# Kernel tuning notes

Hardware: AMD Instinct MI355X
Metric: run time of the kernel (lower is better)

## Reference

```python
import jax, jax.numpy as jnp
import numpy as np

NUM_HEADS = 8
N_POINTS = 9
OFFSET_SCALE = 4.0


def bilinear_sample(fmap_flat, xy, H, W):
    """fmap_flat: (BH, H*W, C) row-major spatial; xy: (BH, S, 2) pixel coords (x, y).
    grid_sample(mode='bilinear', padding_mode='zeros', align_corners=True) equivalent.
    Returns (BH, S, C)."""
    x, y = xy[..., 0], xy[..., 1]
    x0 = jnp.floor(x); y0 = jnp.floor(y)
    x1 = x0 + 1.0;    y1 = y0 + 1.0
    wx1 = x - x0; wx0 = 1.0 - wx1
    wy1 = y - y0; wy0 = 1.0 - wy1

    def corner(xi, yi, wgt):
        valid = (xi >= 0) & (xi <= W - 1) & (yi >= 0) & (yi <= H - 1)
        xi_c = jnp.clip(xi, 0, W - 1).astype(jnp.int32)
        yi_c = jnp.clip(yi, 0, H - 1).astype(jnp.int32)
        idx = yi_c * W + xi_c                                   # (BH, S)
        vals = jnp.take_along_axis(fmap_flat, idx[..., None], axis=1)  # (BH, S, C)
        return vals * (wgt * valid.astype(fmap_flat.dtype))[..., None]

    return (corner(x0, y0, wx0 * wy0) + corner(x1, y0, wx1 * wy0)
            + corner(x0, y1, wx0 * wy1) + corner(x1, y1, wx1 * wy1))


def setup_inputs() -> dict:
    key = jax.random.key(0)
    ks = jax.random.split(key, 10)
    B, N, D = 4, 6400, 256
    Hh, P = NUM_HEADS, N_POINTS
    s = 0.02
    return {
        "x":    jax.random.normal(ks[0], (B, N, D), dtype=jnp.float32),
        "Wq":   jax.random.normal(ks[1], (D, D), dtype=jnp.float32) * s,
        "bq":   jnp.zeros((D,), jnp.float32),
        "Woff": jax.random.normal(ks[2], (Hh * P * 2, D), dtype=jnp.float32) * s,
        "boff": jax.random.normal(ks[3], (Hh * P * 2,), dtype=jnp.float32) * s,
        "Wkv":  jax.random.normal(ks[4], (2 * D, D), dtype=jnp.float32) * s,
        "bkv":  jnp.zeros((2 * D,), jnp.float32),
        "Wout": jax.random.normal(ks[5], (D, D), dtype=jnp.float32) * s,
        "bout": jnp.zeros((D,), jnp.float32),
        "h": 40,
        "w": 160,
    }


def reference(x, Wq, bq, Woff, boff, Wkv, bkv, Wout, bout, h, w):
    B, N, D = x.shape
    H, P = NUM_HEADS, N_POINTS
    hd = D // H

    # queries: (B, H, N, hd)
    q = (x @ Wq.T + bq).reshape(B, N, H, hd).transpose(0, 2, 1, 3)

    # per-query per-head offsets in pixels: (B, N, H, P, 2) (dx, dy)
    offsets = jnp.tanh(x @ Woff.T + boff).reshape(B, N, H, P, 2) * OFFSET_SCALE

    # K/V feature maps via 1x1 conv == per-token linear; split heads, flat spatial
    kv = x @ Wkv.T + bkv                     # (B, N, 2D)
    k = kv[..., :D]
    v = kv[..., D:]
    k_flat = k.reshape(B, N, H, hd).transpose(0, 2, 1, 3).reshape(B * H, N, hd)
    v_flat = v.reshape(B, N, H, hd).transpose(0, 2, 1, 3).reshape(B * H, N, hd)

    # base pixel grid (x, y), row-major over (h, w)
    ys, xs = jnp.meshgrid(jnp.arange(h, dtype=x.dtype), jnp.arange(w, dtype=x.dtype), indexing="ij")
    base_xy = jnp.stack([xs, ys], axis=-1).reshape(N, 2)

    # sampling locations: (B, N, H, P, 2) -> (B*H, N*P, 2)
    sample_xy = base_xy[None, :, None, None, :] + offsets
    sample_xy = sample_xy.transpose(0, 2, 1, 3, 4).reshape(B * H, N * P, 2)

    sampled_k = bilinear_sample(k_flat, sample_xy, h, w).reshape(B, H, N, P, hd)
    sampled_v = bilinear_sample(v_flat, sample_xy, h, w).reshape(B, H, N, P, hd)

    logits = jnp.einsum("bhnd,bhnpd->bhnp", q, sampled_k) * (hd ** -0.5)
    attn = jax.nn.softmax(logits, axis=-1)
    out = jnp.einsum("bhnp,bhnpd->bhnd", attn, sampled_v)   # (B, H, N, hd)
    out = out.transpose(0, 2, 1, 3).reshape(B, N, D)
    return out @ Wout.T + bout
```

## Files before the change

kernel.cpp:

```cpp
#include <hip/hip_runtime.h>
#include <math.h>

#define BSZ    4
#define NTOK   6400
#define DMODEL 256
#define NHEAD  8
#define HDIM   32
#define NPTS   9
#define HSP    40
#define WSP    160
#define KDIM   256
#define MTOT   (BSZ*NTOK)
#define NFUSED 912

typedef short  short8  __attribute__((ext_vector_type(8)));
typedef float  floatx4 __attribute__((ext_vector_type(4)));

__device__ __forceinline__ ushort f2bf(float f) {
    uint u = __float_as_uint(f);
    u = (u + 0x7FFFu + ((u >> 16) & 1u)) >> 16;
    return (ushort)u;
}

__device__ __forceinline__ float fast_tanh(float v) {
    const float e = __expf(2.0f * v);
    return 1.0f - 2.0f / (e + 1.0f);
}

__device__ __forceinline__ void unpack8(uint4 u, float* f) {
    f[0] = __uint_as_float(u.x << 16); f[1] = __uint_as_float(u.x & 0xFFFF0000u);
    f[2] = __uint_as_float(u.y << 16); f[3] = __uint_as_float(u.y & 0xFFFF0000u);
    f[4] = __uint_as_float(u.z << 16); f[5] = __uint_as_float(u.z & 0xFFFF0000u);
    f[6] = __uint_as_float(u.w << 16); f[7] = __uint_as_float(u.w & 0xFFFF0000u);
}

__global__ __launch_bounds__(256) void cast_all(
    const float* __restrict__ x,   const float* __restrict__ Wq,
    const float* __restrict__ Woff,const float* __restrict__ Wkv,
    const float* __restrict__ Wout,
    ushort* __restrict__ xb, ushort* __restrict__ wfused, ushort* __restrict__ woutb)
{
    const int bid = blockIdx.x;
    const float* src; ushort* dst; int base;
    if      (bid < 6400) { src = x;    dst = xb;              base = bid; }
    else if (bid < 6464) { src = Wq;   dst = wfused;          base = bid - 6400; }
    else if (bid < 6500) { src = Woff; dst = wfused + 65536;  base = bid - 6464; }
    else if (bid < 6628) { src = Wkv;  dst = wfused + 102400; base = bid - 6500; }
    else                 { src = Wout; dst = woutb;           base = bid - 6628; }
    const int i = base * 1024 + threadIdx.x * 4;
    float4 v = *(const float4*)(src + i);
    ushort4 o;
    o.x = f2bf(v.x); o.y = f2bf(v.y); o.z = f2bf(v.z); o.w = f2bf(v.w);
    *(ushort4*)(dst + i) = o;
}

template <int MODE>
__global__ __launch_bounds__(256, 3) void gemm_mfma(
    const ushort* __restrict__ Xb,
    const ushort* __restrict__ Wb,
    const float* __restrict__ bq, const float* __restrict__ boff,
    const float* __restrict__ bkv,
    ushort* __restrict__ qb, float* __restrict__ off,
    ushort* __restrict__ kfb, ushort* __restrict__ vfb,
    float* __restrict__ Y)
{
    const int Ncols = (MODE == 0) ? NFUSED : DMODEL;
    __shared__ ushort As[2][128 * 32];
    __shared__ ushort Bs[2][128 * 32];

    const int tid = threadIdx.x;
    const int block_n = blockIdx.x * 128;
    const int block_m = blockIdx.y * 128;
    const int wave = tid >> 6, lane = tid & 63;
    const int wm = (wave >> 1) * 64, wn = (wave & 1) * 64;
    const int l15 = lane & 15, quad = lane >> 4;

    const int r0 = tid >> 2,        q0 = tid & 3;
    const int r1 = (tid + 256) >> 2;
    const int sw0 = ((r0 ^ (r0 >> 2)) & 3);
    const int sw1 = ((r1 ^ (r1 >> 2)) & 3);
    const int lA0 = r0 * 32 + ((q0 ^ sw0) << 3);
    const int lA1 = r1 * 32 + ((q0 ^ sw1) << 3);

    const ushort* gA0 = Xb + (size_t)(block_m + r0) * KDIM + q0 * 8;
    const ushort* gA1 = Xb + (size_t)(block_m + r1) * KDIM + q0 * 8;
    const int bc0 = min(block_n + r0, Ncols - 1);
    const int bc1 = min(block_n + r1, Ncols - 1);
    const ushort* gB0 = Wb + (size_t)bc0 * KDIM + q0 * 8;
    const ushort* gB1 = Wb + (size_t)bc1 * KDIM + q0 * 8;

    const int swf = (l15 & 3) ^ ((l15 >> 2) & 3);
    const int physoff = ((quad ^ swf) << 3);

    floatx4 acc[4][4];
    #pragma unroll
    for (int i = 0; i < 4; ++i)
        #pragma unroll
        for (int j = 0; j < 4; ++j) {
            acc[i][j][0] = 0.f; acc[i][j][1] = 0.f;
            acc[i][j][2] = 0.f; acc[i][j][3] = 0.f;
        }

    {
        uint4 a0 = *(const uint4*)gA0;
        uint4 a1 = *(const uint4*)gA1;
        uint4 b0 = *(const uint4*)gB0;
        uint4 b1 = *(const uint4*)gB1;
        *(uint4*)&As[0][lA0] = a0;  *(uint4*)&As[0][lA1] = a1;
        *(uint4*)&Bs[0][lA0] = b0;  *(uint4*)&Bs[0][lA1] = b1;
    }

    uint4 ra0, ra1, rb0, rb1;
    #pragma unroll
    for (int k8 = 0; k8 < 8; ++k8) {
        __syncthreads();
        if (k8 < 7) {
            const int ko = (k8 + 1) * 32;
            ra0 = *(const uint4*)(gA0 + ko);
            ra1 = *(const uint4*)(gA1 + ko);
            rb0 = *(const uint4*)(gB0 + ko);
            rb1 = *(const uint4*)(gB1 + ko);
        }
        const ushort* Ab = As[k8 & 1];
        const ushort* Bb = Bs[k8 & 1];
        short8 af[4], bfr[4];
        #pragma unroll
        for (int f = 0; f < 4; ++f) {
            af[f]  = *(const short8*)&Ab[(wm + f * 16 + l15) * 32 + physoff];
            bfr[f] = *(const short8*)&Bb[(wn + f * 16 + l15) * 32 + physoff];
        }
        #pragma unroll
        for (int fm = 0; fm < 4; ++fm)
            #pragma unroll
            for (int fn = 0; fn < 4; ++fn)
                acc[fm][fn] = __builtin_amdgcn_mfma_f32_16x16x32_bf16(
                    af[fm], bfr[fn], acc[fm][fn], 0, 0, 0);
        if (k8 < 7) {
            ushort* An = As[(k8 + 1) & 1];
            ushort* Bn = Bs[(k8 + 1) & 1];
            *(uint4*)&An[lA0] = ra0;  *(uint4*)&An[lA1] = ra1;
            *(uint4*)&Bn[lA0] = rb0;  *(uint4*)&Bn[lA1] = rb1;
        }
    }

    float bcol[4]; int colv[4];
    #pragma unroll
    for (int fn = 0; fn < 4; ++fn) {
        const int col = block_n + wn + fn * 16 + l15;
        colv[fn] = col;
        if (MODE == 0) {
            bcol[fn] = (col < 256) ? bq[col]
                     : (col < 400) ? boff[col - 256]
                     : (col < NFUSED) ? bkv[col - 400] : 0.f;
        } else {
            bcol[fn] = bq[col];
        }
    }
    #pragma unroll
    for (int fm = 0; fm < 4; ++fm) {
        #pragma unroll
        for (int r = 0; r < 4; ++r) {
            const int row = block_m + wm + fm * 16 + quad * 4 + r;
            const int b = row / NTOK, n = row % NTOK;
            #pragma unroll
            for (int fn = 0; fn < 4; ++fn) {
                const int col = colv[fn];
                const float val = acc[fm][fn][r] + bcol[fn];
                if (MODE == 1) {
                    Y[(size_t)row * DMODEL + col] = val;
                } else {
                    if (col >= NFUSED) continue;
                    if (col < 256) {
                        qb[(size_t)row * DMODEL + col] = f2bf(val);
                    } else if (col < 400) {
                        off[(size_t)row * 144 + (col - 256)] = fast_tanh(val) * 4.0f;
                    } else {
                        const int kc = col - 400;
                        const int hh = (kc >> 5) & 7, c = kc & 31;
                        const size_t o = (((size_t)(b * NHEAD + hh)) * NTOK + n) * HDIM + c;
                        if (kc < 256) kfb[o] = f2bf(val);
                        else          vfb[o] = f2bf(val);
                    }
                }
            }
        }
    }
}

__global__ __launch_bounds__(256) void deform_attn(
    const ushort* __restrict__ qb,
    const float* __restrict__ off,
    const ushort* __restrict__ kfb,
    const ushort* __restrict__ vfb,
    ushort* __restrict__ attnb)
{
    const int lane = threadIdx.x & 63;
    const int token = blockIdx.x * 8 + (threadIdx.x >> 6) * 2 + (lane >> 5);
    const int h = (lane >> 2) & 7, lc = lane & 3;
    const int b = token / NTOK, n = token % NTOK;

    const uint4 qu = *(const uint4*)(qb + (size_t)token * DMODEL + h * HDIM + lc * 8);
    float q[8]; unpack8(qu, q);

    const float* ob = off + (size_t)token * 144 + h * (NPTS * 2);
    float2 offs[NPTS];
    #pragma unroll
    for (int p = 0; p < NPTS; ++p) offs[p] = *(const float2*)(ob + 2 * p);

    const float bx = (float)(n % WSP), by = (float)(n / WSP);
    const ushort* kb = kfb + (size_t)(b * NHEAD + h) * NTOK * HDIM + lc * 8;
    const ushort* vb = vfb + (size_t)(b * NHEAD + h) * NTOK * HDIM + lc * 8;

    float m = -INFINITY, s = 0.f;
    float o[8];
    #pragma unroll
    for (int c = 0; c < 8; ++c) o[c] = 0.f;

    #pragma unroll
    for (int p = 0; p < NPTS; ++p) {
        const float sx = bx + offs[p].x, sy = by + offs[p].y;
        const float fx0 = floorf(sx), fy0 = floorf(sy);
        const float wx1 = sx - fx0, wx0 = 1.0f - wx1;
        const float wy1 = sy - fy0, wy0 = 1.0f - wy1;
        const int ix0 = (int)fx0, iy0 = (int)fy0;
        const int ix1 = ix0 + 1, iy1 = iy0 + 1;
        const bool vx0 = (ix0 >= 0) & (ix0 <= WSP - 1);
        const bool vx1 = (ix1 >= 0) & (ix1 <= WSP - 1);
        const bool vy0 = (iy0 >= 0) & (iy0 <= HSP - 1);
        const bool vy1 = (iy1 >= 0) & (iy1 <= HSP - 1);
        const int cx0 = min(max(ix0, 0), WSP - 1);
        const int cx1 = min(max(ix1, 0), WSP - 1);
        const int cy0 = min(max(iy0, 0), HSP - 1);
        const int cy1 = min(max(iy1, 0), HSP - 1);
        const float w00 = wx0 * wy0 * (float)(vx0 && vy0);
        const float w10 = wx1 * wy0 * (float)(vx1 && vy0);
        const float w01 = wx0 * wy1 * (float)(vx0 && vy1);
        const float w11 = wx1 * wy1 * (float)(vx1 && vy1);
        const int i00 = (cy0 * WSP + cx0) * HDIM;
        const int i10 = (cy0 * WSP + cx1) * HDIM;
        const int i01 = (cy1 * WSP + cx0) * HDIM;
        const int i11 = (cy1 * WSP + cx1) * HDIM;

        const uint4 ku0 = *(const uint4*)(kb + i00);
        const uint4 ku1 = *(const uint4*)(kb + i10);
        const uint4 ku2 = *(const uint4*)(kb + i01);
        const uint4 ku3 = *(const uint4*)(kb + i11);
        const uint4 vu0 = *(const uint4*)(vb + i00);
        const uint4 vu1 = *(const uint4*)(vb + i10);
        const uint4 vu2 = *(const uint4*)(vb + i01);
        const uint4 vu3 = *(const uint4*)(vb + i11);

        float kc[8], d00 = 0.f, d10 = 0.f, d01 = 0.f, d11 = 0.f;
        unpack8(ku0, kc);
        #pragma unroll
        for (int c = 0; c < 8; ++c) d00 = fmaf(q[c], kc[c], d00);
        unpack8(ku1, kc);
        #pragma unroll
        for (int c = 0; c < 8; ++c) d10 = fmaf(q[c], kc[c], d10);
        unpack8(ku2, kc);
        #pragma unroll
        for (int c = 0; c < 8; ++c) d01 = fmaf(q[c], kc[c], d01);
        unpack8(ku3, kc);
        #pragma unroll
        for (int c = 0; c < 8; ++c) d11 = fmaf(q[c], kc[c], d11);

        float part = w00 * d00 + w10 * d10 + w01 * d01 + w11 * d11;
        part += __shfl_xor(part, 1, 64);
        part += __shfl_xor(part, 2, 64);
        const float l = part * 0.17677669529663687f;

        const float m1 = fmaxf(m, l);
        const float corr = __expf(m - m1);
        const float e = __expf(l - m1);
        s = fmaf(s, corr, e);
        m = m1;

        const float e00 = e * w00, e10 = e * w10, e01 = e * w01, e11 = e * w11;
        float v0[8], v1[8], v2[8], v3[8];
        unpack8(vu0, v0); unpack8(vu1, v1); unpack8(vu2, v2); unpack8(vu3, v3);
        #pragma unroll
        for (int c = 0; c < 8; ++c)
            o[c] = fmaf(o[c], corr,
                        fmaf(e00, v0[c], fmaf(e10, v1[c], fmaf(e01, v2[c], e11 * v3[c]))));
    }

    const float inv = 1.0f / s;
    uint4 ru;
    ru.x = (uint)f2bf(o[0] * inv) | ((uint)f2bf(o[1] * inv) << 16);
    ru.y = (uint)f2bf(o[2] * inv) | ((uint)f2bf(o[3] * inv) << 16);
    ru.z = (uint)f2bf(o[4] * inv) | ((uint)f2bf(o[5] * inv) << 16);
    ru.w = (uint)f2bf(o[6] * inv) | ((uint)f2bf(o[7] * inv) << 16);
    *(uint4*)(attnb + (size_t)token * DMODEL + h * HDIM + lc * 8) = ru;
}

extern "C" void kernel_launch(void* const* d_in, const int* in_sizes, int n_in,
                              void* d_out, int out_size, void* d_ws, size_t ws_size,
                              hipStream_t stream) {
    const float* x    = (const float*)d_in[0];
    const float* Wq   = (const float*)d_in[1];
    const float* bq   = (const float*)d_in[2];
    const float* Woff = (const float*)d_in[3];
    const float* boff = (const float*)d_in[4];
    const float* Wkv  = (const float*)d_in[5];
    const float* bkv  = (const float*)d_in[6];
    const float* Wout = (const float*)d_in[7];
    const float* bout = (const float*)d_in[8];

    ushort* xb     = (ushort*)d_ws;
    ushort* qb     = xb + (size_t)MTOT * DMODEL;
    float*  off    = (float*)(qb + (size_t)MTOT * DMODEL);
    ushort* kfb    = (ushort*)(off + (size_t)MTOT * 144);
    ushort* vfb    = kfb + (size_t)MTOT * DMODEL;
    ushort* wfused = vfb + (size_t)MTOT * DMODEL;
    ushort* woutb  = wfused + NFUSED * KDIM;
    ushort* attnb  = xb;

    cast_all<<<dim3(6692), dim3(256), 0, stream>>>(x, Wq, Woff, Wkv, Wout,
                                                   xb, wfused, woutb);
    gemm_mfma<0><<<dim3(8, 200), dim3(256), 0, stream>>>(
        xb, wfused, bq, boff, bkv, qb, off, kfb, vfb, nullptr);
    deform_attn<<<dim3(3200), dim3(256), 0, stream>>>(qb, off, kfb, vfb, attnb);
    gemm_mfma<1><<<dim3(2, 200), dim3(256), 0, stream>>>(
        attnb, woutb, bout, nullptr, nullptr, nullptr, nullptr, nullptr, nullptr,
        (float*)d_out);
}
```

Measured before the change: 218.1 us.

## Remap deform_attn to two lanes per head with packed float2 math and no online max

Each head's 32-dim channel slice is now handled by 2 lanes of 16 channels instead of 4 lanes of 8. That halves the cross-lane shuffles per point and doubles tokens per block, so the grid shrinks to 1600 blocks. The math uses float2 vectors so the compiler can emit packed FMA instructions. The online-softmax max tracking is dropped, which relies on the logits staying small enough not to overflow exp. In exchange, register pressure rises and each lane issues twice as many gather loads, which may hurt occupancy.

```diff
diff --git a/kernel.cpp b/kernel.cpp
--- a/kernel.cpp
+++ b/kernel.cpp
@@ -15,6 +15,7 @@
 
 typedef short  short8  __attribute__((ext_vector_type(8)));
 typedef float  floatx4 __attribute__((ext_vector_type(4)));
+typedef float  float2v __attribute__((ext_vector_type(2)));
 
 __device__ __forceinline__ ushort f2bf(float f) {
     uint u = __float_as_uint(f);
@@ -27,11 +28,11 @@
     return 1.0f - 2.0f / (e + 1.0f);
 }
 
-__device__ __forceinline__ void unpack8(uint4 u, float* f) {
-    f[0] = __uint_as_float(u.x << 16); f[1] = __uint_as_float(u.x & 0xFFFF0000u);
-    f[2] = __uint_as_float(u.y << 16); f[3] = __uint_as_float(u.y & 0xFFFF0000u);
-    f[4] = __uint_as_float(u.z << 16); f[5] = __uint_as_float(u.z & 0xFFFF0000u);
-    f[6] = __uint_as_float(u.w << 16); f[7] = __uint_as_float(u.w & 0xFFFF0000u);
+__device__ __forceinline__ float2v up2(uint u) {
+    float2v r;
+    r.x = __uint_as_float(u << 16);
+    r.y = __uint_as_float(u & 0xFFFF0000u);
+    return r;
 }
 
 __global__ __launch_bounds__(256) void cast_all(
@@ -195,12 +196,17 @@
     ushort* __restrict__ attnb)
 {
     const int lane = threadIdx.x & 63;
-    const int token = blockIdx.x * 8 + (threadIdx.x >> 6) * 2 + (lane >> 5);
-    const int h = (lane >> 2) & 7, lc = lane & 3;
+    const int token = blockIdx.x * 16 + (threadIdx.x >> 6) * 4 + (lane >> 4);
+    const int h = (lane >> 1) & 7;
+    const int j = lane & 1;
     const int b = token / NTOK, n = token % NTOK;
 
-    const uint4 qu = *(const uint4*)(qb + (size_t)token * DMODEL + h * HDIM + lc * 8);
-    float q[8]; unpack8(qu, q);
+    const ushort* qp = qb + (size_t)token * DMODEL + h * HDIM + j * 16;
+    const uint4 qu0 = *(const uint4*)qp;
+    const uint4 qu1 = *(const uint4*)(qp + 8);
+    float2v q2[8];
+    q2[0] = up2(qu0.x); q2[1] = up2(qu0.y); q2[2] = up2(qu0.z); q2[3] = up2(qu0.w);
+    q2[4] = up2(qu1.x); q2[5] = up2(qu1.y); q2[6] = up2(qu1.z); q2[7] = up2(qu1.w);
 
     const float* ob = off + (size_t)token * 144 + h * (NPTS * 2);
     float2 offs[NPTS];
@@ -208,13 +214,13 @@
     for (int p = 0; p < NPTS; ++p) offs[p] = *(const float2*)(ob + 2 * p);
 
     const float bx = (float)(n % WSP), by = (float)(n / WSP);
-    const ushort* kb = kfb + (size_t)(b * NHEAD + h) * NTOK * HDIM + lc * 8;
-    const ushort* vb = vfb + (size_t)(b * NHEAD + h) * NTOK * HDIM + lc * 8;
-
-    float m = -INFINITY, s = 0.f;
-    float o[8];
-    #pragma unroll
-    for (int c = 0; c < 8; ++c) o[c] = 0.f;
+    const ushort* kb = kfb + (size_t)(b * NHEAD + h) * NTOK * HDIM + j * 16;
+    const ushort* vb = vfb + (size_t)(b * NHEAD + h) * NTOK * HDIM + j * 16;
+
+    float s = 0.f;
+    float2v o2[8];
+    #pragma unroll
+    for (int c = 0; c < 8; ++c) o2[c] = (float2v)0.f;
 
     #pragma unroll
     for (int p = 0; p < NPTS; ++p) {
@@ -241,56 +247,82 @@
         const int i01 = (cy1 * WSP + cx0) * HDIM;
         const int i11 = (cy1 * WSP + cx1) * HDIM;
 
-        const uint4 ku0 = *(const uint4*)(kb + i00);
-        const uint4 ku1 = *(const uint4*)(kb + i10);
-        const uint4 ku2 = *(const uint4*)(kb + i01);
-        const uint4 ku3 = *(const uint4*)(kb + i11);
-        const uint4 vu0 = *(const uint4*)(vb + i00);
-        const uint4 vu1 = *(const uint4*)(vb + i10);
-        const uint4 vu2 = *(const uint4*)(vb + i01);
-        const uint4 vu3 = *(const uint4*)(vb + i11);
-
-        float kc[8], d00 = 0.f, d10 = 0.f, d01 = 0.f, d11 = 0.f;
-        unpack8(ku0, kc);
-        #pragma unroll
-        for (int c = 0; c < 8; ++c) d00 = fmaf(q[c], kc[c], d00);
-        unpack8(ku1, kc);
-        #pragma unroll
-        for (int c = 0; c < 8; ++c) d10 = fmaf(q[c], kc[c], d10);
-        unpack8(ku2, kc);
-        #pragma unroll
-        for (int c = 0; c < 8; ++c) d01 = fmaf(q[c], kc[c], d01);
-        unpack8(ku3, kc);
-        #pragma unroll
-        for (int c = 0; c < 8; ++c) d11 = fmaf(q[c], kc[c], d11);
-
-        float part = w00 * d00 + w10 * d10 + w01 * d01 + w11 * d11;
+        const uint4 ka0 = *(const uint4*)(kb + i00);
+        const uint4 ka1 = *(const uint4*)(kb + i00 + 8);
+        const uint4 kb0 = *(const uint4*)(kb + i10);
+        const uint4 kb1 = *(const uint4*)(kb + i10 + 8);
+        const uint4 kc0 = *(const uint4*)(kb + i01);
+        const uint4 kc1 = *(const uint4*)(kb + i01 + 8);
+        const uint4 kd0 = *(const uint4*)(kb + i11);
+        const uint4 kd1 = *(const uint4*)(kb + i11 + 8);
+
+        float2v d00 = (float2v)0.f, d10 = (float2v)0.f;
+        float2v d01 = (float2v)0.f, d11 = (float2v)0.f;
+        d00 += q2[0] * up2(ka0.x); d00 += q2[1] * up2(ka0.y);
+        d00 += q2[2] * up2(ka0.z); d00 += q2[3] * up2(ka0.w);
+        d00 += q2[4] * up2(ka1.x); d00 += q2[5] * up2(ka1.y);
+        d00 += q2[6] * up2(ka1.z); d00 += q2[7] * up2(ka1.w);
+        d10 += q2[0] * up2(kb0.x); d10 += q2[1] * up2(kb0.y);
+        d10 += q2[2] * up2(kb0.z); d10 += q2[3] * up2(kb0.w);
+        d10 += q2[4] * up2(kb1.x); d10 += q2[5] * up2(kb1.y);
+        d10 += q2[6] * up2(kb1.z); d10 += q2[7] * up2(kb1.w);
+        d01 += q2[0] * up2(kc0.x); d01 += q2[1] * up2(kc0.y);
+        d01 += q2[2] * up2(kc0.z); d01 += q2[3] * up2(kc0.w);
+        d01 += q2[4] * up2(kc1.x); d01 += q2[5] * up2(kc1.y);
+        d01 += q2[6] * up2(kc1.z); d01 += q2[7] * up2(kc1.w);
+        d11 += q2[0] * up2(kd0.x); d11 += q2[1] * up2(kd0.y);
+        d11 += q2[2] * up2(kd0.z); d11 += q2[3] * up2(kd0.w);
+        d11 += q2[4] * up2(kd1.x); d11 += q2[5] * up2(kd1.y);
+        d11 += q2[6] * up2(kd1.z); d11 += q2[7] * up2(kd1.w);
+
+        const float2v dsum = w00 * d00 + w10 * d10 + w01 * d01 + w11 * d11;
+        float part = dsum.x + dsum.y;
         part += __shfl_xor(part, 1, 64);
-        part += __shfl_xor(part, 2, 64);
-        const float l = part * 0.17677669529663687f;
-
-        const float m1 = fmaxf(m, l);
-        const float corr = __expf(m - m1);
-        const float e = __expf(l - m1);
-        s = fmaf(s, corr, e);
-        m = m1;
+        const float e = __expf(part * 0.17677669529663687f);
+        s += e;
 
         const float e00 = e * w00, e10 = e * w10, e01 = e * w01, e11 = e * w11;
-        float v0[8], v1[8], v2[8], v3[8];
-        unpack8(vu0, v0); unpack8(vu1, v1); unpack8(vu2, v2); unpack8(vu3, v3);
-        #pragma unroll
-        for (int c = 0; c < 8; ++c)
-            o[c] = fmaf(o[c], corr,
-                        fmaf(e00, v0[c], fmaf(e10, v1[c], fmaf(e01, v2[c], e11 * v3[c]))));
+
+        const uint4 va0 = *(const uint4*)(vb + i00);
+        const uint4 va1 = *(const uint4*)(vb + i00 + 8);
+        const uint4 vb0 = *(const uint4*)(vb + i10);
+        const uint4 vb1 = *(const uint4*)(vb + i10 + 8);
+        const uint4 vc0 = *(const uint4*)(vb + i01);
+        const uint4 vc1 = *(const uint4*)(vb + i01 + 8);
+        const uint4 vd0 = *(const uint4*)(vb + i11);
+        const uint4 vd1 = *(const uint4*)(vb + i11 + 8);
+
+        o2[0] += e00 * up2(va0.x); o2[1] += e00 * up2(va0.y);
+        o2[2] += e00 * up2(va0.z); o2[3] += e00 * up2(va0.w);
+        o2[4] += e00 * up2(va1.x); o2[5] += e00 * up2(va1.y);
+        o2[6] += e00 * up2(va1.z); o2[7] += e00 * up2(va1.w);
+        o2[0] += e10 * up2(vb0.x); o2[1] += e10 * up2(vb0.y);
+        o2[2] += e10 * up2(vb0.z); o2[3] += e10 * up2(vb0.w);
+        o2[4] += e10 * up2(vb1.x); o2[5] += e10 * up2(vb1.y);
+        o2[6] += e10 * up2(vb1.z); o2[7] += e10 * up2(vb1.w);
+        o2[0] += e01 * up2(vc0.x); o2[1] += e01 * up2(vc0.y);
+        o2[2] += e01 * up2(vc0.z); o2[3] += e01 * up2(vc0.w);
+        o2[4] += e01 * up2(vc1.x); o2[5] += e01 * up2(vc1.y);
+        o2[6] += e01 * up2(vc1.z); o2[7] += e01 * up2(vc1.w);
+        o2[0] += e11 * up2(vd0.x); o2[1] += e11 * up2(vd0.y);
+        o2[2] += e11 * up2(vd0.z); o2[3] += e11 * up2(vd0.w);
+        o2[4] += e11 * up2(vd1.x); o2[5] += e11 * up2(vd1.y);
+        o2[6] += e11 * up2(vd1.z); o2[7] += e11 * up2(vd1.w);
     }
 
     const float inv = 1.0f / s;
-    uint4 ru;
-    ru.x = (uint)f2bf(o[0] * inv) | ((uint)f2bf(o[1] * inv) << 16);
-    ru.y = (uint)f2bf(o[2] * inv) | ((uint)f2bf(o[3] * inv) << 16);
-    ru.z = (uint)f2bf(o[4] * inv) | ((uint)f2bf(o[5] * inv) << 16);
-    ru.w = (uint)f2bf(o[6] * inv) | ((uint)f2bf(o[7] * inv) << 16);
-    *(uint4*)(attnb + (size_t)token * DMODEL + h * HDIM + lc * 8) = ru;
+    uint4 r0, r1;
+    r0.x = (uint)f2bf(o2[0].x * inv) | ((uint)f2bf(o2[0].y * inv) << 16);
+    r0.y = (uint)f2bf(o2[1].x * inv) | ((uint)f2bf(o2[1].y * inv) << 16);
+    r0.z = (uint)f2bf(o2[2].x * inv) | ((uint)f2bf(o2[2].y * inv) << 16);
+    r0.w = (uint)f2bf(o2[3].x * inv) | ((uint)f2bf(o2[3].y * inv) << 16);
+    r1.x = (uint)f2bf(o2[4].x * inv) | ((uint)f2bf(o2[4].y * inv) << 16);
+    r1.y = (uint)f2bf(o2[5].x * inv) | ((uint)f2bf(o2[5].y * inv) << 16);
+    r1.z = (uint)f2bf(o2[6].x * inv) | ((uint)f2bf(o2[6].y * inv) << 16);
+    r1.w = (uint)f2bf(o2[7].x * inv) | ((uint)f2bf(o2[7].y * inv) << 16);
+    ushort* op = attnb + (size_t)token * DMODEL + h * HDIM + j * 16;
+    *(uint4*)op = r0;
+    *(uint4*)(op + 8) = r1;
 }
 
 extern "C" void kernel_launch(void* const* d_in, const int* in_sizes, int n_in,
@@ -319,7 +351,7 @@
                                                    xb, wfused, woutb);
     gemm_mfma<0><<<dim3(8, 200), dim3(256), 0, stream>>>(
         xb, wfused, bq, boff, bkv, qb, off, kfb, vfb, nullptr);
-    deform_attn<<<dim3(3200), dim3(256), 0, stream>>>(qb, off, kfb, vfb, attnb);
+    deform_attn<<<dim3(1600), dim3(256), 0, stream>>>(qb, off, kfb, vfb, attnb);
     gemm_mfma<1><<<dim3(2, 200), dim3(256), 0, stream>>>(
         attnb, woutb, bout, nullptr, nullptr, nullptr, nullptr, nullptr, nullptr,
         (float*)d_out);
```

New measurement: 238.0 us. +9.1%, slower.
